# Kernel tuning notes

Hardware: AMD Instinct MI355X
Metric: run time of the kernel (lower is better)

## Reference

```python
import jax, jax.numpy as jnp
import numpy as np

POOL_K = {56: 8, 28: 4, 14: 2, 7: 1}


def _maxpool(x, k):
    # kernel == stride maxpool via reshape-max
    if k == 1:
        return x
    B, C, H, W = x.shape
    return x.reshape(B, C, H // k, k, W // k, k).max(axis=(3, 5))


def _scale(act):
    # act: [B, C, H0, W0] -> pooled [B, C, 7, 7]
    B, C, H0, W0 = act.shape
    p = _maxpool(act, POOL_K[H0]).reshape(B, C, -1)  # [B, C, HW], HW=49
    # heatmap[i,j,e,f] = sum_c p[i,c,e] * p[j,c,f]  -> [B, B, HW, HW]
    heat = jax.nn.softmax(jnp.einsum('ice,jcf->ijef', p, p), axis=-1)
    # out[i,j,e,c] = sum_f heat[i,j,e,f] * p[j,c,f]  -> [B, B, HW, C]
    out = jnp.einsum('ijef,jcf->ijec', heat, p)
    return out, heat


def setup_inputs() -> dict:
    key = jax.random.key(0)
    k1, k2, k3, k4 = jax.random.split(key, 4)
    B = 16
    return {
        'act1': jax.random.normal(k1, (B, 256, 56, 56), dtype=jnp.float32),
        'act2': jax.random.normal(k2, (B, 512, 28, 28), dtype=jnp.float32),
        'act3': jax.random.normal(k3, (B, 1024, 14, 14), dtype=jnp.float32),
        'act4': jax.random.normal(k4, (B, 2048, 7, 7), dtype=jnp.float32),
    }


def reference(act1, act2, act3, act4):
    outs_heats = [_scale(a) for a in (act1, act2, act3, act4)]
    outs = tuple(o for o, _ in outs_heats)
    heats = tuple(h for _, h in outs_heats)
    return outs + heats
```

## Files before the change

### kernel.cpp

```cpp
#include <hip/hip_runtime.h>
#include <hip/hip_bf16.h>
#include <cstdint>
#include <cstddef>


typedef __attribute__((ext_vector_type(8))) short s16x8;
typedef __attribute__((ext_vector_type(4))) float f32x4;
typedef __attribute__((ext_vector_type(4))) uint32_t u32x4;

#define SPART 802816

__device__ __forceinline__ unsigned short f2bf(float x) {
    uint32_t u = __float_as_uint(x);
    uint32_t r = (u + 0x7fff + ((u >> 16) & 1)) >> 16;
    return (unsigned short)r;
}
__device__ __forceinline__ float bf2f(unsigned short b) {
    return __uint_as_float(((uint32_t)b) << 16);
}
__device__ __forceinline__ void gll16(const void* g, void* l) {
    __builtin_amdgcn_global_load_lds(
        (const __attribute__((address_space(1))) uint32_t*)g,
        (__attribute__((address_space(3))) uint32_t*)l, 16, 0, 0);
}

struct PoolParams {
    const float* act[4];
    unsigned short* Pk[4];
    unsigned short* Vb[4];
    int C[4], H[4], k[4], G[4], cum[5];
};

__global__ __launch_bounds__(256) void pool_all_kernel(PoolParams pp) {
    __shared__ alignas(16) float plane[3136];
    int b = blockIdx.x, s = 0;
    while (b >= pp.cum[s + 1]) s++;
    const int rem = b - pp.cum[s];
    const int C = pp.C[s], H = pp.H[s], k = pp.k[s], G = pp.G[s];
    const int HW = H * H;
    const int nblk_c = C / G;
    const int i  = rem / nblk_c;
    const int c0 = (rem % nblk_c) * G;
    unsigned short* __restrict__ Pk = pp.Pk[s];
    unsigned short* __restrict__ Vb = pp.Vb[s];

    const float4* src4 = reinterpret_cast<const float4*>(pp.act[s] + ((size_t)i * C + c0) * HW);
    float4* plane4 = reinterpret_cast<float4*>(plane);
    for (int idx = threadIdx.x; idx < (G * HW) >> 2; idx += 256)
        plane4[idx] = src4[idx];
    __syncthreads();
    for (int idx = threadIdx.x; idx < G * 49; idx += 256) {
        const int e = idx / G, g = idx % G;
        const int eh = e / 7, ew = e % 7;
        const float* ppl = plane + g * HW + (eh * k) * H + ew * k;
        float m = -INFINITY;
        for (int dy = 0; dy < k; ++dy)
            for (int dx = 0; dx < k; ++dx)
                m = fmaxf(m, ppl[dy * H + dx]);
        const int c = c0 + g;
        const unsigned short hb = f2bf(m);
        const unsigned short lb = f2bf(m - bf2f(hb));
        const size_t pk = (((size_t)(c >> 2) * 896) + (size_t)i * 56 + e) * 8 + ((c & 3) * 2);
        *reinterpret_cast<uint32_t*>(&Pk[pk]) = (uint32_t)hb | ((uint32_t)lb << 16);
        const size_t vb = (((size_t)i * 8 + (e >> 3)) * C + c) * 8 + (e & 7);
        Vb[vb] = hb;
    }
    for (int idx = threadIdx.x; idx < 7 * G; idx += 256) {
        const int e = 49 + idx / G, g = idx % G, c = c0 + g;
        const size_t pk = (((size_t)(c >> 2) * 896) + (size_t)i * 56 + e) * 8 + ((c & 3) * 2);
        *reinterpret_cast<uint32_t*>(&Pk[pk]) = 0;
    }
    for (int idx = threadIdx.x; idx < 15 * G; idx += 256) {
        const int e = 49 + idx / G, g = idx % G, c = c0 + g;
        const size_t vb = (((size_t)i * 8 + (e >> 3)) * C + c) * 8 + (e & 7);
        Vb[vb] = 0;
    }
}

struct GramParams {
    const unsigned short* Pk[4];
    float* S[4];
    int Kblk[4];
    int cum[5];
};

__global__ __launch_bounds__(256) void gram_kernel(GramParams g) {
    __shared__ short lsA[2][4096];
    __shared__ short lsB[2][4096];
    int b = blockIdx.x, s = 0;
    while (b >= g.cum[s + 1]) s++;
    const int rem = b - g.cum[s];
    const int p = rem / 49, t = rem % 49;
    const int bi = t / 7, bj = t % 7;
    const int Kb = g.Kblk[s];
    const int kg0 = p * (Kb >> 3);
    const unsigned short* __restrict__ Pk = g.Pk[s];
    float* __restrict__ S = g.S[s] + (size_t)p * SPART;

    const int tid = threadIdx.x, lane = tid & 63, w = tid >> 6;
    const int wm = (w >> 1) * 64, wn = (w & 1) * 64;

    f32x4 acc[4][4];
    #pragma unroll
    for (int u = 0; u < 4; ++u)
        #pragma unroll
        for (int v = 0; v < 4; ++v)
            acc[u][v] = (f32x4){0.f, 0.f, 0.f, 0.f};

    const int half = lane >> 4, r16 = lane & 15;
    const int nt = Kb >> 5;

#define GSTAGE(buf, it) do {                                                        \
        const int kq_ = kg0 + (it) * 4 + w;                                         \
        const char* ga_ = (const char*)Pk + ((size_t)kq_ * 896 + bi * 128) * 16 + lane * 16; \
        const char* gb_ = (const char*)Pk + ((size_t)kq_ * 896 + bj * 128) * 16 + lane * 16; \
        gll16(ga_,        (char*)lsA[buf] + w * 2048);                              \
        gll16(ga_ + 1024, (char*)lsA[buf] + w * 2048 + 1024);                       \
        gll16(gb_,        (char*)lsB[buf] + w * 2048);                              \
        gll16(gb_ + 1024, (char*)lsB[buf] + w * 2048 + 1024);                       \
    } while (0)

    GSTAGE(0, 0);
    asm volatile("s_waitcnt vmcnt(0)" ::: "memory");
    __builtin_amdgcn_s_barrier();

    int cur = 0;
    for (int it = 0; it < nt; ++it) {
        if (it + 1 < nt) GSTAGE(cur ^ 1, it + 1);
        s16x8 av[4], bv[4], cv[4];
        #pragma unroll
        for (int u = 0; u < 4; ++u) {
            av[u] = *reinterpret_cast<const s16x8*>(&lsA[cur][((half * 128) + wm + 16 * u + r16) * 8]);
            union { u32x4 u4; s16x8 s8; } ub, uc;
            ub.u4 = *reinterpret_cast<const u32x4*>(&lsB[cur][((half * 128) + wn + 16 * u + r16) * 8]);
            uc.u4 = (ub.u4 >> 16) | (ub.u4 << 16);
            bv[u] = ub.s8;
            cv[u] = uc.s8;
        }
        #pragma unroll
        for (int u = 0; u < 4; ++u)
            #pragma unroll
            for (int v = 0; v < 4; ++v) {
                acc[u][v] = __builtin_amdgcn_mfma_f32_16x16x32_bf16(av[u], bv[v], acc[u][v], 0, 0, 0);
                acc[u][v] = __builtin_amdgcn_mfma_f32_16x16x32_bf16(av[u], cv[v], acc[u][v], 0, 0, 0);
            }
        __builtin_amdgcn_sched_barrier(0);
        asm volatile("s_waitcnt vmcnt(0)" ::: "memory");
        __builtin_amdgcn_s_barrier();
        cur ^= 1;
    }
#undef GSTAGE

    const int rowb = bi * 128 + wm + (lane >> 4) * 4;
    const int colb = bj * 128 + wn + (lane & 15);
    #pragma unroll
    for (int u = 0; u < 4; ++u)
        #pragma unroll
        for (int v = 0; v < 4; ++v)
            #pragma unroll
            for (int rg = 0; rg < 4; ++rg)
                S[(size_t)(rowb + 16 * u + rg) * 896 + colb + 16 * v] = acc[u][v][rg];
}

struct SoftParams {
    const float* S[4];
    float* heat[4];
    unsigned short* Hb[4];
    int np[4];
};

__global__ __launch_bounds__(256) void softmax_kernel(SoftParams sp) {
    const int grp = (blockIdx.x * 256 + threadIdx.x) >> 4;
    const int l = threadIdx.x & 15;
    const int s = grp / 12544;
    const int rem = grp % 12544;
    const int i = rem / 784;
    const int j = (rem / 49) % 16;
    const int e = rem % 49;
    const float* __restrict__ Sb = sp.S[s];
    const int np = sp.np[s];
    const size_t rowoff = ((size_t)(i * 56 + e)) * 896 + j * 56;

    float v[4];
    #pragma unroll
    for (int t = 0; t < 4; ++t) {
        const int f = l + t * 16;
        float x = -INFINITY;
        if (f < 49) {
            x = 0.f;
            for (int p = 0; p < np; ++p) x += Sb[(size_t)p * SPART + rowoff + f];
        }
        v[t] = x;
    }
    float m = fmaxf(fmaxf(v[0], v[1]), fmaxf(v[2], v[3]));
    #pragma unroll
    for (int d = 1; d < 16; d <<= 1) m = fmaxf(m, __shfl_xor(m, d, 16));
    float ex[4], sum = 0.f;
    #pragma unroll
    for (int t = 0; t < 4; ++t) {
        const int f = l + t * 16;
        ex[t] = (f < 49) ? __expf(v[t] - m) : 0.f;
        sum += ex[t];
    }
    #pragma unroll
    for (int d = 1; d < 16; d <<= 1) sum += __shfl_xor(sum, d, 16);
    const float inv = 1.f / sum;

    float* hrow = sp.heat[s] + (((size_t)(i * 16 + j)) * 49 + e) * 49;
    unsigned short* __restrict__ Hb = sp.Hb[s];
    const size_t hbrow = (size_t)i * 56 + e;
    #pragma unroll
    for (int t = 0; t < 4; ++t) {
        const int f = l + t * 16;
        const float hv = (f < 49) ? ex[t] * inv : 0.f;
        if (f < 49) hrow[f] = hv;
        Hb[(((size_t)j * 8 + (f >> 3)) * 896 + hbrow) * 8 + (f & 7)] = f2bf(hv);
    }
}

struct PvParams {
    const unsigned short* Hb[4];
    const unsigned short* Vb[4];
    float* out[4];
    int C[4];
    int cum[5];
};

__global__ __launch_bounds__(256) void pv_kernel(PvParams pv) {
    __shared__ short lsA[8 * 128 * 8];
    __shared__ short lsB[8 * 128 * 8];
    int b = blockIdx.x, s = 0;
    while (b >= pv.cum[s + 1]) s++;
    int rem = b - pv.cum[s];
    const int C = pv.C[s], nct = C >> 7;
    const int j = rem / (7 * nct); rem %= 7 * nct;
    const int rt = rem / nct, ct = rem % nct;
    const int tid = threadIdx.x, lane = tid & 63, w = tid >> 6;
    const int wm = (w >> 1) * 64, wn = (w & 1) * 64;
    const unsigned short* __restrict__ Hb = pv.Hb[s];
    const unsigned short* __restrict__ Vb = pv.Vb[s];

    #pragma unroll
    for (int q = 0; q < 2; ++q) {
        const int kq = w + q * 4;
        const char* ga = (const char*)Hb + ((size_t)(j * 8 + kq) * 896 + rt * 128) * 16 + lane * 16;
        const char* gb = (const char*)Vb + ((size_t)(j * 8 + kq) * C + ct * 128) * 16 + lane * 16;
        gll16(ga,        (char*)lsA + kq * 2048);
        gll16(ga + 1024, (char*)lsA + kq * 2048 + 1024);
        gll16(gb,        (char*)lsB + kq * 2048);
        gll16(gb + 1024, (char*)lsB + kq * 2048 + 1024);
    }
    __syncthreads();

    f32x4 acc[4][4];
    #pragma unroll
    for (int u = 0; u < 4; ++u)
        #pragma unroll
        for (int v = 0; v < 4; ++v)
            acc[u][v] = (f32x4){0.f, 0.f, 0.f, 0.f};

    const int r16 = lane & 15;
    #pragma unroll
    for (int ks = 0; ks < 2; ++ks) {
        const int half = ks * 4 + (lane >> 4);
        s16x8 av[4], bv[4];
        #pragma unroll
        for (int u = 0; u < 4; ++u) {
            av[u] = *reinterpret_cast<const s16x8*>(&lsA[((half * 128) + wm + 16 * u + r16) * 8]);
            bv[u] = *reinterpret_cast<const s16x8*>(&lsB[((half * 128) + wn + 16 * u + r16) * 8]);
        }
        #pragma unroll
        for (int u = 0; u < 4; ++u)
            #pragma unroll
            for (int v = 0; v < 4; ++v)
                acc[u][v] = __builtin_amdgcn_mfma_f32_16x16x32_bf16(av[u], bv[v], acc[u][v], 0, 0, 0);
    }

    #pragma unroll
    for (int u = 0; u < 4; ++u) {
        const int mb = rt * 128 + wm + 16 * u + (lane >> 4) * 4;
        #pragma unroll
        for (int rg = 0; rg < 4; ++rg) {
            const int mm = mb + rg;
            const int ii = mm / 56, e = mm % 56;
            if (e < 49) {
                float* orow = pv.out[s] + (((size_t)(ii * 16 + j)) * 49 + e) * C + ct * 128 + (lane & 15);
                #pragma unroll
                for (int v = 0; v < 4; ++v)
                    orow[wn + 16 * v] = acc[u][v][rg];
            }
        }
    }
}

extern "C" void kernel_launch(void* const* d_in, const int* in_sizes, int n_in,
                              void* d_out, int out_size, void* d_ws, size_t ws_size,
                              hipStream_t stream) {
    const int Cs[4] = {256, 512, 1024, 2048};
    const int Hs[4] = {56, 28, 14, 7};
    const int ks[4] = {8, 4, 2, 1};
    const int Gs[4] = {1, 4, 16, 64};

    char* w0 = (char*)d_ws;
    size_t off = 0;
    unsigned short *Pk[4], *Vb[4], *Hb[4];
    for (int s = 0; s < 4; ++s) { Pk[s] = (unsigned short*)(w0 + off); off += (size_t)3584 * Cs[s]; }
    for (int s = 0; s < 4; ++s) { Vb[s] = (unsigned short*)(w0 + off); off += (size_t)2048 * Cs[s]; }
    for (int s = 0; s < 4; ++s) { Hb[s] = (unsigned short*)(w0 + off); off += (size_t)1835008; }

    int np[4] = {1, 2, 2, 4};
    {
        size_t need = off;
        for (int s = 0; s < 4; ++s) need += (size_t)np[s] * SPART * 4;
        if (ws_size < need) { np[0] = np[1] = np[2] = np[3] = 1; }
    }
    float* Sp[4];
    for (int s = 0; s < 4; ++s) { Sp[s] = (float*)(w0 + off); off += (size_t)np[s] * SPART * 4; }

    float* out = (float*)d_out;
    const size_t o1 = 0;
    const size_t o2 = o1 + (size_t)256 * 49 * 256;
    const size_t o3 = o2 + (size_t)256 * 49 * 512;
    const size_t o4 = o3 + (size_t)256 * 49 * 1024;
    const size_t h1 = o4 + (size_t)256 * 49 * 2048;
    const size_t h2 = h1 + (size_t)256 * 2401;
    const size_t h3 = h2 + (size_t)256 * 2401;
    const size_t h4 = h3 + (size_t)256 * 2401;
    float* heat[4] = {out + h1, out + h2, out + h3, out + h4};
    float* outs[4] = {out + o1, out + o2, out + o3, out + o4};

    PoolParams pp;
    pp.cum[0] = 0;
    for (int s = 0; s < 4; ++s) {
        pp.act[s] = (const float*)d_in[s];
        pp.Pk[s] = Pk[s]; pp.Vb[s] = Vb[s];
        pp.C[s] = Cs[s]; pp.H[s] = Hs[s]; pp.k[s] = ks[s]; pp.G[s] = Gs[s];
        pp.cum[s + 1] = pp.cum[s] + 16 * (Cs[s] / Gs[s]);
    }
    pool_all_kernel<<<pp.cum[4], 256, 0, stream>>>(pp);

    GramParams g;
    g.cum[0] = 0;
    for (int s = 0; s < 4; ++s) {
        g.Pk[s] = Pk[s];
        g.S[s] = Sp[s];
        g.Kblk[s] = 2 * Cs[s] / np[s];
        g.cum[s + 1] = g.cum[s] + np[s] * 49;
    }
    gram_kernel<<<g.cum[4], 256, 0, stream>>>(g);

    SoftParams sp;
    for (int s = 0; s < 4; ++s) {
        sp.S[s] = Sp[s]; sp.heat[s] = heat[s]; sp.Hb[s] = Hb[s]; sp.np[s] = np[s];
    }
    softmax_kernel<<<3136, 256, 0, stream>>>(sp);

    PvParams pv;
    pv.cum[0] = 0;
    for (int s = 0; s < 4; ++s) {
        pv.Hb[s] = Hb[s]; pv.Vb[s] = Vb[s]; pv.out[s] = outs[s]; pv.C[s] = Cs[s];
        pv.cum[s + 1] = pv.cum[s] + 16 * 7 * (Cs[s] >> 7);
    }
    pv_kernel<<<pv.cum[4], 256, 0, stream>>>(pv);
}
```

Before: 132.1 us.

## Fuse softmax into PV kernel, loop over column tiles, restructure pooling writes

Softmax is computed inside the PV kernel and written straight to shared memory as bf16, which removes the separate softmax launch and the Hb global round trip. Each block now loops over all channel tiles with double-buffered V loads, scheduling the largest scale first. The pooling kernel stages maxima in shared memory so the Pk and Vb stores, including zero padding, can each use coalesced index orders. The cost is far fewer PV blocks (448), each doing serial work over up to 16 tiles, which risks lower parallelism and load imbalance.

Result: slower. 164.8 us (+24.7%).

```diff
diff --git a/kernel.cpp b/kernel.cpp
--- a/kernel.cpp
+++ b/kernel.cpp
@@ -33,6 +33,7 @@
 
 __global__ __launch_bounds__(256) void pool_all_kernel(PoolParams pp) {
     __shared__ alignas(16) float plane[3136];
+    __shared__ float smax[4096];
     int b = blockIdx.x, s = 0;
     while (b >= pp.cum[s + 1]) s++;
     const int rem = b - pp.cum[s];
@@ -49,31 +50,34 @@
     for (int idx = threadIdx.x; idx < (G * HW) >> 2; idx += 256)
         plane4[idx] = src4[idx];
     __syncthreads();
-    for (int idx = threadIdx.x; idx < G * 49; idx += 256) {
-        const int e = idx / G, g = idx % G;
-        const int eh = e / 7, ew = e % 7;
-        const float* ppl = plane + g * HW + (eh * k) * H + ew * k;
-        float m = -INFINITY;
-        for (int dy = 0; dy < k; ++dy)
-            for (int dx = 0; dx < k; ++dx)
-                m = fmaxf(m, ppl[dy * H + dx]);
-        const int c = c0 + g;
+
+    for (int idx = threadIdx.x; idx < (G << 6); idx += 256) {
+        const int g = idx >> 6, e = idx & 63;
+        float m = 0.f;
+        if (e < 49) {
+            const int eh = e / 7, ew = e % 7;
+            const float* ppl = plane + g * HW + (eh * k) * H + ew * k;
+            m = -INFINITY;
+            for (int dy = 0; dy < k; ++dy)
+                for (int dx = 0; dx < k; ++dx)
+                    m = fmaxf(m, ppl[dy * H + dx]);
+        }
+        smax[idx] = m;
+    }
+    __syncthreads();
+
+    for (int idx = threadIdx.x; idx < G * 56; idx += 256) {
+        const int e = idx / G, g = idx % G, c = c0 + g;
+        const float m = (e < 49) ? smax[(g << 6) + e] : 0.f;
         const unsigned short hb = f2bf(m);
         const unsigned short lb = f2bf(m - bf2f(hb));
         const size_t pk = (((size_t)(c >> 2) * 896) + (size_t)i * 56 + e) * 8 + ((c & 3) * 2);
         *reinterpret_cast<uint32_t*>(&Pk[pk]) = (uint32_t)hb | ((uint32_t)lb << 16);
+    }
+    for (int idx = threadIdx.x; idx < (G << 6); idx += 256) {
+        const int g = idx >> 6, e = idx & 63, c = c0 + g;
         const size_t vb = (((size_t)i * 8 + (e >> 3)) * C + c) * 8 + (e & 7);
-        Vb[vb] = hb;
-    }
-    for (int idx = threadIdx.x; idx < 7 * G; idx += 256) {
-        const int e = 49 + idx / G, g = idx % G, c = c0 + g;
-        const size_t pk = (((size_t)(c >> 2) * 896) + (size_t)i * 56 + e) * 8 + ((c & 3) * 2);
-        *reinterpret_cast<uint32_t*>(&Pk[pk]) = 0;
-    }
-    for (int idx = threadIdx.x; idx < 15 * G; idx += 256) {
-        const int e = 49 + idx / G, g = idx % G, c = c0 + g;
-        const size_t vb = (((size_t)i * 8 + (e >> 3)) * C + c) * 8 + (e & 7);
-        Vb[vb] = 0;
+        Vb[vb] = f2bf(smax[idx]);
     }
 }
 
@@ -162,135 +166,147 @@
                 S[(size_t)(rowb + 16 * u + rg) * 896 + colb + 16 * v] = acc[u][v][rg];
 }
 
-struct SoftParams {
+struct Pv2Params {
     const float* S[4];
+    const unsigned short* Vb[4];
     float* heat[4];
-    unsigned short* Hb[4];
-    int np[4];
-};
-
-__global__ __launch_bounds__(256) void softmax_kernel(SoftParams sp) {
-    const int grp = (blockIdx.x * 256 + threadIdx.x) >> 4;
-    const int l = threadIdx.x & 15;
-    const int s = grp / 12544;
-    const int rem = grp % 12544;
-    const int i = rem / 784;
-    const int j = (rem / 49) % 16;
-    const int e = rem % 49;
-    const float* __restrict__ Sb = sp.S[s];
-    const int np = sp.np[s];
-    const size_t rowoff = ((size_t)(i * 56 + e)) * 896 + j * 56;
-
-    float v[4];
-    #pragma unroll
-    for (int t = 0; t < 4; ++t) {
-        const int f = l + t * 16;
-        float x = -INFINITY;
-        if (f < 49) {
-            x = 0.f;
-            for (int p = 0; p < np; ++p) x += Sb[(size_t)p * SPART + rowoff + f];
-        }
-        v[t] = x;
-    }
-    float m = fmaxf(fmaxf(v[0], v[1]), fmaxf(v[2], v[3]));
-    #pragma unroll
-    for (int d = 1; d < 16; d <<= 1) m = fmaxf(m, __shfl_xor(m, d, 16));
-    float ex[4], sum = 0.f;
-    #pragma unroll
-    for (int t = 0; t < 4; ++t) {
-        const int f = l + t * 16;
-        ex[t] = (f < 49) ? __expf(v[t] - m) : 0.f;
-        sum += ex[t];
-    }
-    #pragma unroll
-    for (int d = 1; d < 16; d <<= 1) sum += __shfl_xor(sum, d, 16);
-    const float inv = 1.f / sum;
-
-    float* hrow = sp.heat[s] + (((size_t)(i * 16 + j)) * 49 + e) * 49;
-    unsigned short* __restrict__ Hb = sp.Hb[s];
-    const size_t hbrow = (size_t)i * 56 + e;
-    #pragma unroll
-    for (int t = 0; t < 4; ++t) {
-        const int f = l + t * 16;
-        const float hv = (f < 49) ? ex[t] * inv : 0.f;
-        if (f < 49) hrow[f] = hv;
-        Hb[(((size_t)j * 8 + (f >> 3)) * 896 + hbrow) * 8 + (f & 7)] = f2bf(hv);
-    }
-}
-
-struct PvParams {
-    const unsigned short* Hb[4];
-    const unsigned short* Vb[4];
     float* out[4];
-    int C[4];
+    int C[4], np[4];
+    int sord[4];
     int cum[5];
 };
 
-__global__ __launch_bounds__(256) void pv_kernel(PvParams pv) {
-    __shared__ short lsA[8 * 128 * 8];
-    __shared__ short lsB[8 * 128 * 8];
-    int b = blockIdx.x, s = 0;
-    while (b >= pv.cum[s + 1]) s++;
-    int rem = b - pv.cum[s];
-    const int C = pv.C[s], nct = C >> 7;
-    const int j = rem / (7 * nct); rem %= 7 * nct;
-    const int rt = rem / nct, ct = rem % nct;
-    const int tid = threadIdx.x, lane = tid & 63, w = tid >> 6;
+__global__ __launch_bounds__(256) void pv2_kernel(Pv2Params pv) {
+    __shared__ short lsH[8192];
+    __shared__ short lsV[2][8192];
+    int b = blockIdx.x, q = 0;
+    while (b >= pv.cum[q + 1]) q++;
+    const int s = pv.sord[q];
+    int rem = b - pv.cum[q];
+    const int j = rem / 7, rt = rem % 7;
+    const int C = pv.C[s], nct = C >> 7, np = pv.np[s];
+    const int tid = threadIdx.x;
+
+    {
+        const float* __restrict__ Sb = pv.S[s];
+        float* __restrict__ heat = pv.heat[s];
+        const int grp = tid >> 4, l = tid & 15;
+        for (int pass = 0; pass < 8; ++pass) {
+            const int r = pass * 16 + grp;
+            const int R = rt * 128 + r;
+            const int i = R / 56, e = R % 56;
+            float hv[4] = {0.f, 0.f, 0.f, 0.f};
+            if (e < 49) {
+                float v[4];
+                #pragma unroll
+                for (int t = 0; t < 4; ++t) {
+                    const int f = l + 16 * t;
+                    float x = -INFINITY;
+                    if (f < 49) {
+                        x = 0.f;
+                        for (int p = 0; p < np; ++p)
+                            x += Sb[(size_t)p * SPART + (size_t)R * 896 + j * 56 + f];
+                    }
+                    v[t] = x;
+                }
+                float m = fmaxf(fmaxf(v[0], v[1]), fmaxf(v[2], v[3]));
+                #pragma unroll
+                for (int d = 1; d < 16; d <<= 1) m = fmaxf(m, __shfl_xor(m, d, 16));
+                float sum = 0.f;
+                #pragma unroll
+                for (int t = 0; t < 4; ++t) {
+                    const int f = l + 16 * t;
+                    hv[t] = (f < 49) ? __expf(v[t] - m) : 0.f;
+                    sum += hv[t];
+                }
+                #pragma unroll
+                for (int d = 1; d < 16; d <<= 1) sum += __shfl_xor(sum, d, 16);
+                const float inv = 1.f / sum;
+                float* hrow = heat + (((size_t)(i * 16 + j)) * 49 + e) * 49;
+                #pragma unroll
+                for (int t = 0; t < 4; ++t) {
+                    const int f = l + 16 * t;
+                    hv[t] *= inv;
+                    if (f < 49) hrow[f] = hv[t];
+                }
+            }
+            #pragma unroll
+            for (int t = 0; t < 4; ++t) {
+                const int f = l + 16 * t;
+                lsH[((f >> 3) << 10) + r * 8 + (f & 7)] = f2bf(hv[t]);
+            }
+        }
+    }
+
+    const int lane = tid & 63, w = tid >> 6;
     const int wm = (w >> 1) * 64, wn = (w & 1) * 64;
-    const unsigned short* __restrict__ Hb = pv.Hb[s];
+    const int r16 = lane & 15;
     const unsigned short* __restrict__ Vb = pv.Vb[s];
-
-    #pragma unroll
-    for (int q = 0; q < 2; ++q) {
-        const int kq = w + q * 4;
-        const char* ga = (const char*)Hb + ((size_t)(j * 8 + kq) * 896 + rt * 128) * 16 + lane * 16;
-        const char* gb = (const char*)Vb + ((size_t)(j * 8 + kq) * C + ct * 128) * 16 + lane * 16;
-        gll16(ga,        (char*)lsA + kq * 2048);
-        gll16(ga + 1024, (char*)lsA + kq * 2048 + 1024);
-        gll16(gb,        (char*)lsB + kq * 2048);
-        gll16(gb + 1024, (char*)lsB + kq * 2048 + 1024);
-    }
+    float* __restrict__ outp = pv.out[s];
+
+#define VSTAGE(buf, ct_) do {                                                       \
+        _Pragma("unroll")                                                           \
+        for (int qq = 0; qq < 2; ++qq) {                                            \
+            const int kq_ = w + qq * 4;                                             \
+            const char* gb_ = (const char*)Vb + ((size_t)(j * 8 + kq_) * C + (ct_) * 128) * 16 + lane * 16; \
+            gll16(gb_,        (char*)lsV[buf] + kq_ * 2048);                        \
+            gll16(gb_ + 1024, (char*)lsV[buf] + kq_ * 2048 + 1024);                 \
+        }                                                                           \
+    } while (0)
+
+    VSTAGE(0, 0);
     __syncthreads();
 
-    f32x4 acc[4][4];
-    #pragma unroll
-    for (int u = 0; u < 4; ++u)
-        #pragma unroll
-        for (int v = 0; v < 4; ++v)
-            acc[u][v] = (f32x4){0.f, 0.f, 0.f, 0.f};
-
-    const int r16 = lane & 15;
-    #pragma unroll
-    for (int ks = 0; ks < 2; ++ks) {
-        const int half = ks * 4 + (lane >> 4);
-        s16x8 av[4], bv[4];
+    int cur = 0;
+    for (int ct = 0; ct < nct; ++ct) {
+        f32x4 acc[4][4];
+        #pragma unroll
+        for (int u = 0; u < 4; ++u)
+            #pragma unroll
+            for (int v = 0; v < 4; ++v)
+                acc[u][v] = (f32x4){0.f, 0.f, 0.f, 0.f};
+
+        #pragma unroll
+        for (int ks = 0; ks < 2; ++ks) {
+            const int half = ks * 4 + (lane >> 4);
+            s16x8 av[4], bv[4];
+            #pragma unroll
+            for (int u = 0; u < 4; ++u) {
+                av[u] = *reinterpret_cast<const s16x8*>(&lsH[((half << 10)) + (wm + 16 * u + r16) * 8]);
+                bv[u] = *reinterpret_cast<const s16x8*>(&lsV[cur][((half << 10)) + (wn + 16 * u + r16) * 8]);
+            }
+            #pragma unroll
+            for (int u = 0; u < 4; ++u)
+                #pragma unroll
+                for (int v = 0; v < 4; ++v)
+                    acc[u][v] = __builtin_amdgcn_mfma_f32_16x16x32_bf16(av[u], bv[v], acc[u][v], 0, 0, 0);
+        }
+
+        if (ct + 1 < nct) VSTAGE(cur ^ 1, ct + 1);
+
         #pragma unroll
         for (int u = 0; u < 4; ++u) {
-            av[u] = *reinterpret_cast<const s16x8*>(&lsA[((half * 128) + wm + 16 * u + r16) * 8]);
-            bv[u] = *reinterpret_cast<const s16x8*>(&lsB[((half * 128) + wn + 16 * u + r16) * 8]);
-        }
-        #pragma unroll
-        for (int u = 0; u < 4; ++u)
-            #pragma unroll
-            for (int v = 0; v < 4; ++v)
-                acc[u][v] = __builtin_amdgcn_mfma_f32_16x16x32_bf16(av[u], bv[v], acc[u][v], 0, 0, 0);
-    }
-
-    #pragma unroll
-    for (int u = 0; u < 4; ++u) {
-        const int mb = rt * 128 + wm + 16 * u + (lane >> 4) * 4;
-        #pragma unroll
-        for (int rg = 0; rg < 4; ++rg) {
-            const int mm = mb + rg;
-            const int ii = mm / 56, e = mm % 56;
-            if (e < 49) {
-                float* orow = pv.out[s] + (((size_t)(ii * 16 + j)) * 49 + e) * C + ct * 128 + (lane & 15);
-                #pragma unroll
-                for (int v = 0; v < 4; ++v)
-                    orow[wn + 16 * v] = acc[u][v][rg];
-            }
-        }
-    }
+            const int mb = rt * 128 + wm + 16 * u + (lane >> 4) * 4;
+            #pragma unroll
+            for (int rg = 0; rg < 4; ++rg) {
+                const int mm = mb + rg;
+                const int ii = mm / 56, e = mm % 56;
+                if (e < 49) {
+                    float* orow = outp + (((size_t)(ii * 16 + j)) * 49 + e) * C + ct * 128 + r16;
+                    #pragma unroll
+                    for (int v = 0; v < 4; ++v)
+                        orow[wn + 16 * v] = acc[u][v][rg];
+                }
+            }
+        }
+
+        if (ct + 1 < nct) {
+            __builtin_amdgcn_sched_barrier(0);
+            asm volatile("s_waitcnt vmcnt(48)\n\ts_barrier" ::: "memory");
+        }
+        cur ^= 1;
+    }
+#undef VSTAGE
 }
 
 extern "C" void kernel_launch(void* const* d_in, const int* in_sizes, int n_in,
@@ -303,10 +319,9 @@
 
     char* w0 = (char*)d_ws;
     size_t off = 0;
-    unsigned short *Pk[4], *Vb[4], *Hb[4];
+    unsigned short *Pk[4], *Vb[4];
     for (int s = 0; s < 4; ++s) { Pk[s] = (unsigned short*)(w0 + off); off += (size_t)3584 * Cs[s]; }
     for (int s = 0; s < 4; ++s) { Vb[s] = (unsigned short*)(w0 + off); off += (size_t)2048 * Cs[s]; }
-    for (int s = 0; s < 4; ++s) { Hb[s] = (unsigned short*)(w0 + off); off += (size_t)1835008; }
 
     int np[4] = {1, 2, 2, 4};
     {
@@ -349,17 +364,14 @@
     }
     gram_kernel<<<g.cum[4], 256, 0, stream>>>(g);
 
-    SoftParams sp;
+    Pv2Params pv;
+    pv.sord[0] = 3; pv.sord[1] = 2; pv.sord[2] = 1; pv.sord[3] = 0;
+    pv.cum[0] = 0;
+    for (int q = 0; q < 4; ++q) pv.cum[q + 1] = pv.cum[q] + 16 * 7;
     for (int s = 0; s < 4; ++s) {
-        sp.S[s] = Sp[s]; sp.heat[s] = heat[s]; sp.Hb[s] = Hb[s]; sp.np[s] = np[s];
-    }
-    softmax_kernel<<<3136, 256, 0, stream>>>(sp);
-
-    PvParams pv;
-    pv.cum[0] = 0;
-    for (int s = 0; s < 4; ++s) {
-        pv.Hb[s] = Hb[s]; pv.Vb[s] = Vb[s]; pv.out[s] = outs[s]; pv.C[s] = Cs[s];
-        pv.cum[s + 1] = pv.cum[s] + 16 * 7 * (Cs[s] >> 7);
-    }
-    pv_kernel<<<pv.cum[4], 256, 0, stream>>>(pv);
-}
+        pv.S[s] = Sp[s]; pv.Vb[s] = Vb[s];
+        pv.heat[s] = heat[s]; pv.out[s] = outs[s];
+        pv.C[s] = Cs[s]; pv.np[s] = np[s];
+    }
+    pv2_kernel<<<pv.cum[4], 256, 0, stream>>>(pv);
+}
```

## Add XCD-aware block swizzle to all kernels and coalesce V writes in pooling

Applied to the files above, without the earlier changes.

Remaps block indices in the pool, gram, softmax and PV kernels so that consecutive logical blocks land on the same XCD. The aim is better L2 locality across the eight chiplets. The pooling kernel also writes the bf16 V tensor in a separate loop indexed by channel-major lanes, so the stores are more contiguous, at the cost of recomputing the max-pool for V. Both changes keep the math the same.

New measurement: 163.7 us. 23.9% more time.

```diff
diff --git a/kernel.cpp b/kernel.cpp
--- a/kernel.cpp
+++ b/kernel.cpp
@@ -22,6 +22,11 @@
     __builtin_amdgcn_global_load_lds(
         (const __attribute__((address_space(1))) uint32_t*)g,
         (__attribute__((address_space(3))) uint32_t*)l, 16, 0, 0);
+}
+__device__ __forceinline__ int xcd_swz(int b, int nwg) {
+    const int q = nwg >> 3, r = nwg & 7;
+    const int x = b & 7, t = b >> 3;
+    return (x < r ? x * (q + 1) : r * (q + 1) + (x - r) * q) + t;
 }
 
 struct PoolParams {
@@ -33,7 +38,7 @@
 
 __global__ __launch_bounds__(256) void pool_all_kernel(PoolParams pp) {
     __shared__ alignas(16) float plane[3136];
-    int b = blockIdx.x, s = 0;
+    int b = xcd_swz(blockIdx.x, pp.cum[4]), s = 0;
     while (b >= pp.cum[s + 1]) s++;
     const int rem = b - pp.cum[s];
     const int C = pp.C[s], H = pp.H[s], k = pp.k[s], G = pp.G[s];
@@ -49,6 +54,7 @@
     for (int idx = threadIdx.x; idx < (G * HW) >> 2; idx += 256)
         plane4[idx] = src4[idx];
     __syncthreads();
+
     for (int idx = threadIdx.x; idx < G * 49; idx += 256) {
         const int e = idx / G, g = idx % G;
         const int eh = e / 7, ew = e % 7;
@@ -62,18 +68,25 @@
         const unsigned short lb = f2bf(m - bf2f(hb));
         const size_t pk = (((size_t)(c >> 2) * 896) + (size_t)i * 56 + e) * 8 + ((c & 3) * 2);
         *reinterpret_cast<uint32_t*>(&Pk[pk]) = (uint32_t)hb | ((uint32_t)lb << 16);
-        const size_t vb = (((size_t)i * 8 + (e >> 3)) * C + c) * 8 + (e & 7);
-        Vb[vb] = hb;
     }
     for (int idx = threadIdx.x; idx < 7 * G; idx += 256) {
         const int e = 49 + idx / G, g = idx % G, c = c0 + g;
         const size_t pk = (((size_t)(c >> 2) * 896) + (size_t)i * 56 + e) * 8 + ((c & 3) * 2);
         *reinterpret_cast<uint32_t*>(&Pk[pk]) = 0;
     }
-    for (int idx = threadIdx.x; idx < 15 * G; idx += 256) {
-        const int e = 49 + idx / G, g = idx % G, c = c0 + g;
+    for (int idx = threadIdx.x; idx < (G << 6); idx += 256) {
+        const int g = idx >> 6, e = idx & 63, c = c0 + g;
+        float m = 0.f;
+        if (e < 49) {
+            const int eh = e / 7, ew = e % 7;
+            const float* ppl = plane + g * HW + (eh * k) * H + ew * k;
+            m = -INFINITY;
+            for (int dy = 0; dy < k; ++dy)
+                for (int dx = 0; dx < k; ++dx)
+                    m = fmaxf(m, ppl[dy * H + dx]);
+        }
         const size_t vb = (((size_t)i * 8 + (e >> 3)) * C + c) * 8 + (e & 7);
-        Vb[vb] = 0;
+        Vb[vb] = f2bf(m);
     }
 }
 
@@ -87,7 +100,7 @@
 __global__ __launch_bounds__(256) void gram_kernel(GramParams g) {
     __shared__ short lsA[2][4096];
     __shared__ short lsB[2][4096];
-    int b = blockIdx.x, s = 0;
+    int b = xcd_swz(blockIdx.x, g.cum[4]), s = 0;
     while (b >= g.cum[s + 1]) s++;
     const int rem = b - g.cum[s];
     const int p = rem / 49, t = rem % 49;
@@ -170,7 +183,8 @@
 };
 
 __global__ __launch_bounds__(256) void softmax_kernel(SoftParams sp) {
-    const int grp = (blockIdx.x * 256 + threadIdx.x) >> 4;
+    const int sb = xcd_swz(blockIdx.x, 3136);
+    const int grp = (sb * 256 + threadIdx.x) >> 4;
     const int l = threadIdx.x & 15;
     const int s = grp / 12544;
     const int rem = grp % 12544;
@@ -229,7 +243,7 @@
 __global__ __launch_bounds__(256) void pv_kernel(PvParams pv) {
     __shared__ short lsA[8 * 128 * 8];
     __shared__ short lsB[8 * 128 * 8];
-    int b = blockIdx.x, s = 0;
+    int b = xcd_swz(blockIdx.x, pv.cum[4]), s = 0;
     while (b >= pv.cum[s + 1]) s++;
     int rem = b - pv.cum[s];
     const int C = pv.C[s], nct = C >> 7;
```
